# Kernel tuning notes

Hardware: AMD Instinct MI355X
Metric: run time of the kernel (lower is better)

## Reference

```python
import jax, jax.numpy as jnp
import numpy as np

C = 64   # in_channels
KS = 3   # kernel_size


def _wconv(p, W1, b1, W2, b2, W3, b3):
    # 1x1 conv stack: 3 -> 64 -> 256 -> C*KS*KS, ReLU between
    h = jax.nn.relu(jnp.einsum('oc,bchw->bohw', W1, p) + b1[None, :, None, None])
    h = jax.nn.relu(jnp.einsum('oc,bchw->bohw', W2, h) + b2[None, :, None, None])
    h = jnp.einsum('oc,bchw->bohw', W3, h) + b3[None, :, None, None]
    return h  # [1, C*KS*KS, ho, wo]


def setup_inputs() -> dict:
    key = jax.random.key(0)
    k = jax.random.split(key, 8)
    bs, hi, wi = 2, 128, 128
    ho, wo = 512, 512
    x = jax.random.normal(k[0], (bs, C, hi, wi), jnp.float32)
    poseMap = jax.random.normal(k[1], (1, 3, ho, wo), jnp.float32)
    interMapY = jax.random.randint(k[2], (ho, wo), 0, hi)
    interMapX = jax.random.randint(k[3], (ho, wo), 0, wi)
    W1 = jax.random.normal(k[4], (64, 3), jnp.float32) * 0.1
    b1 = jnp.zeros((64,), jnp.float32)
    W2 = jax.random.normal(k[5], (256, 64), jnp.float32) * 0.05
    b2 = jnp.zeros((256,), jnp.float32)
    W3 = jax.random.normal(k[6], (C * KS * KS, 256), jnp.float32) * 0.05
    b3 = jnp.zeros((C * KS * KS,), jnp.float32)
    return {'x': x, 'poseMap': poseMap, 'W1': W1, 'b1': b1, 'W2': W2, 'b2': b2,
            'W3': W3, 'b3': b3, 'interMapY': interMapY, 'interMapX': interMapX}


def reference(x, poseMap, W1, b1, W2, b2, W3, b3, interMapY, interMapX):
    bs, c, hi, wi = x.shape
    ho, wo = interMapY.shape
    # kernel prediction branch (poseMap is detached in the original)
    w = _wconv(jax.lax.stop_gradient(poseMap), W1, b1, W2, b2, W3, b3)
    w = w.reshape(C, KS * KS, ho, wo)
    sw = jax.nn.softmax(w, axis=1)  # softmax over the KS*KS taps
    # unfold(x, KS, padding=KS//2) tap k corresponds to xp[:, :, i + k//KS, j + k%KS]
    pad = KS // 2
    xp = jnp.pad(x, ((0, 0), (0, 0), (pad, pad), (pad, pad)))
    out = jnp.zeros((bs, C, ho, wo), x.dtype)
    for k in range(KS * KS):  # fixed small loop over taps; fuses gather+weight+reduce
        dy, dx = k // KS, k % KS
        g = xp[:, :, interMapY + dy, interMapX + dx]  # [bs, C, ho, wo] paired gather
        out = out + g * sw[None, :, k]  # sw[:, k] -> [C, ho, wo]
    return out
```

## Files before the change

### kernel.cpp

```cpp
#include <hip/hip_runtime.h>
#include <math.h>

#define HO 512
#define WO 512
#define HI 128
#define WI 128
#define CC 64
#define BS 2
#define NPX 64
#define NT 256

#define W2P_ELEMS (16 * 2 * 64 * 8)
#define W3P_ELEMS (36 * 8 * 64 * 8)
#define XT_ELEM_OFF (W2P_ELEMS + W3P_ELEMS)
#define XT_FLOATS (130 * 130 * 128)

typedef __attribute__((ext_vector_type(8))) short short8;
typedef __attribute__((ext_vector_type(4))) float float4v;

__device__ __forceinline__ unsigned short f2bf(float f) {
    unsigned u = __builtin_bit_cast(unsigned, f);
    unsigned r = (u + 0x7FFFu + ((u >> 16) & 1u)) >> 16;
    return (unsigned short)r;
}

__global__ void prepack_zw(const float* __restrict__ W2,
                           const float* __restrict__ W3,
                           unsigned short* __restrict__ wsp,
                           float* __restrict__ xt) {
    const int total = W2P_ELEMS + W3P_ELEMS;
    for (int idx = blockIdx.x * blockDim.x + threadIdx.x; idx < total;
         idx += gridDim.x * blockDim.x) {
        float v;
        if (idx < W2P_ELEMS) {
            int j = idx & 7, lane = (idx >> 3) & 63, rest = idx >> 9;
            int ks = rest & 1, nt = rest >> 1;
            int n = nt * 16 + (lane & 15);
            int k = ks * 32 + (lane >> 4) * 8 + j;
            v = W2[n * 64 + k];
        } else {
            int i2 = idx - W2P_ELEMS;
            int j = i2 & 7, lane = (i2 >> 3) & 63, rest = i2 >> 9;
            int ks = rest & 7, nt = rest >> 3;
            int tap = nt >> 2, ct = nt & 3;
            int row = (ct * 16 + (lane & 15)) * 9 + tap;
            int k = ks * 32 + (lane >> 4) * 8 + j;
            v = W3[row * 256 + k];
        }
        wsp[idx] = f2bf(v);
    }
    float4v z = {0.f, 0.f, 0.f, 0.f};
    float4v* xt4 = (float4v*)xt;
    for (int i = blockIdx.x * blockDim.x + threadIdx.x; i < XT_FLOATS / 4;
         i += gridDim.x * blockDim.x)
        xt4[i] = z;
}

__global__ void prepack_x(const float* __restrict__ x, float* __restrict__ xt) {
    const int tid = blockIdx.x * blockDim.x + threadIdx.x;
    const int pos = tid & 16383;
    const int g   = tid >> 14;
    const int h = pos >> 7, w = pos & 127;
    const float* src = x + pos;
    float4v v0, v1;
    #pragma unroll
    for (int j = 0; j < 4; ++j) v0[j] = src[(size_t)(g * 8 + j) * (HI * WI)];
    #pragma unroll
    for (int j = 0; j < 4; ++j) v1[j] = src[(size_t)(g * 8 + 4 + j) * (HI * WI)];
    float* dst = xt + ((h + 1) * 130 + (w + 1)) * 128 + g * 8;
    *(float4v*)dst = v0;
    *(float4v*)(dst + 4) = v1;
}

__global__ __launch_bounds__(NT, 3)
void fused_main(const float* __restrict__ xt, const float* __restrict__ pose,
                const float* __restrict__ W1, const float* __restrict__ b1,
                const float* __restrict__ b2, const float* __restrict__ b3,
                const int* __restrict__ iY, const int* __restrict__ iX,
                const unsigned short* __restrict__ wsp,
                float* __restrict__ out)
{
    __shared__ char smem[33792 + 17408 + 768 + 512];
    unsigned short (*sH2)[264] = (unsigned short (*)[264])&smem[0];
    unsigned short (*sH1)[72]  = (unsigned short (*)[72])&smem[33792];
    float (*sOut)[2][16][68]   = (float (*)[2][16][68])&smem[33792];
    float (*sP)[NPX]           = (float (*)[NPX])&smem[51200];
    int* sIY                   = (int*)&smem[51968];
    int* sIX                   = (int*)&smem[52224];

    const int t = threadIdx.x;
    const int pixBase = blockIdx.x * NPX;
    const int y  = pixBase / WO;
    const int x0 = pixBase % WO;

    if (t < 192) sP[t >> 6][t & 63] = pose[(t >> 6) * (HO * WO) + pixBase + (t & 63)];
    if (t < 64) sIY[t] = iY[pixBase + t];
    else if (t < 128) sIX[t - 64] = iX[pixBase + t - 64];
    __syncthreads();

    {
        const int p  = t & 63;
        const int og = t >> 6;
        const float p0 = sP[0][p], p1 = sP[1][p], p2 = sP[2][p];
        #pragma unroll
        for (int i = 0; i < 16; i += 2) {
            const int o = og * 16 + i;
            float a0 = fmaf(W1[o * 3 + 2], p2, fmaf(W1[o * 3 + 1], p1, fmaf(W1[o * 3 + 0], p0, b1[o])));
            float a1 = fmaf(W1[o * 3 + 5], p2, fmaf(W1[o * 3 + 4], p1, fmaf(W1[o * 3 + 3], p0, b1[o + 1])));
            a0 = fmaxf(a0, 0.f); a1 = fmaxf(a1, 0.f);
            unsigned pack = (unsigned)f2bf(a0) | ((unsigned)f2bf(a1) << 16);
            *(unsigned*)&sH1[p][o] = pack;
        }
    }
    __syncthreads();

    const int wv = t >> 6, l = t & 63, lm = l & 15, lq = l >> 4;
    const int m0 = wv * 16;

    {
        short8 a0 = *(const short8*)&sH1[m0 + lm][0  + lq * 8];
        short8 a1 = *(const short8*)&sH1[m0 + lm][32 + lq * 8];
        const short8* w2f = (const short8*)wsp;
        #pragma unroll 4
        for (int nt = 0; nt < 16; ++nt) {
            float4v acc = {0.f, 0.f, 0.f, 0.f};
            short8 bf0 = w2f[(nt * 2 + 0) * 64 + l];
            short8 bf1 = w2f[(nt * 2 + 1) * 64 + l];
            acc = __builtin_amdgcn_mfma_f32_16x16x32_bf16(a0, bf0, acc, 0, 0, 0);
            acc = __builtin_amdgcn_mfma_f32_16x16x32_bf16(a1, bf1, acc, 0, 0, 0);
            const float bv = b2[nt * 16 + lm];
            #pragma unroll
            for (int r = 0; r < 4; ++r)
                sH2[m0 + lq * 4 + r][nt * 16 + lm] = f2bf(fmaxf(acc[r] + bv, 0.f));
        }
    }
    __syncthreads();

    int pbase[4];
    #pragma unroll
    for (int r = 0; r < 4; ++r) {
        const int p = m0 + lq * 4 + r;
        pbase[r] = ((sIY[p] + 1) * 130 + (sIX[p] + 1)) * 128;
    }
    const int koff[9] = {-131 * 128, -130 * 128, -129 * 128,
                         -1 * 128,   0,          1 * 128,
                         129 * 128,  130 * 128,  131 * 128};
    const short8* w3f = (const short8*)(wsp + W2P_ELEMS);

    for (int ct = 0; ct < 4; ++ct) {
        float4v accs[9];
        #pragma unroll
        for (int tap = 0; tap < 9; ++tap) accs[tap] = (float4v){0.f, 0.f, 0.f, 0.f};

        #pragma unroll 2
        for (int ks = 0; ks < 8; ++ks) {
            short8 a = *(const short8*)&sH2[m0 + lm][ks * 32 + lq * 8];
            #pragma unroll
            for (int tap = 0; tap < 9; ++tap) {
                short8 b = w3f[(((tap << 2) | ct) * 8 + ks) * 64 + l];
                accs[tap] = __builtin_amdgcn_mfma_f32_16x16x32_bf16(a, b, accs[tap], 0, 0, 0);
            }
        }

        const int c = ct * 16 + lm;
        float bv[9];
        #pragma unroll
        for (int tap = 0; tap < 9; ++tap) bv[tap] = b3[c * 9 + tap];

        float ob0[4], ob1[4];
        #pragma unroll
        for (int r = 0; r < 4; ++r) {
            float lg[9];
            #pragma unroll
            for (int tap = 0; tap < 9; ++tap) lg[tap] = accs[tap][r] + bv[tap];
            float mx = lg[0];
            #pragma unroll
            for (int tap = 1; tap < 9; ++tap) mx = fmaxf(mx, lg[tap]);
            const float* xb = xt + pbase[r] + c;
            float s = 0.f, o0 = 0.f, o1 = 0.f;
            #pragma unroll
            for (int tap = 0; tap < 9; ++tap) {
                const float ev = __expf(lg[tap] - mx);
                s += ev;
                o0 = fmaf(ev, xb[koff[tap]], o0);
                o1 = fmaf(ev, xb[koff[tap] + 64], o1);
            }
            const float inv = 1.f / s;
            ob0[r] = o0 * inv;
            ob1[r] = o1 * inv;
        }

        float (*so)[16][68] = sOut[ct & 1];
        *(float4v*)&so[0][lm][m0 + lq * 4] = (float4v){ob0[0], ob0[1], ob0[2], ob0[3]};
        *(float4v*)&so[1][lm][m0 + lq * 4] = (float4v){ob1[0], ob1[1], ob1[2], ob1[3]};
        __syncthreads();

        const int row = t >> 3;
        const int b   = row >> 4, ch = row & 15;
        const int seg = (t & 7) * 8;
        float4v v0 = *(float4v*)&so[b][ch][seg];
        float4v v1 = *(float4v*)&so[b][ch][seg + 4];
        float* op = out + (((size_t)(b * CC + ct * 16 + ch) * HO) + y) * WO + x0 + seg;
        *(float4v*)op = v0;
        *(float4v*)(op + 4) = v1;
    }
}

extern "C" void kernel_launch(void* const* d_in, const int* in_sizes, int n_in,
                              void* d_out, int out_size, void* d_ws, size_t ws_size,
                              hipStream_t stream) {
    const float* x    = (const float*)d_in[0];
    const float* pose = (const float*)d_in[1];
    const float* W1   = (const float*)d_in[2];
    const float* b1   = (const float*)d_in[3];
    const float* W2   = (const float*)d_in[4];
    const float* b2   = (const float*)d_in[5];
    const float* W3   = (const float*)d_in[6];
    const float* b3   = (const float*)d_in[7];
    const int*   iY   = (const int*)d_in[8];
    const int*   iX   = (const int*)d_in[9];
    float* out = (float*)d_out;
    unsigned short* wsp = (unsigned short*)d_ws;
    float* xt = (float*)((char*)d_ws + XT_ELEM_OFF * sizeof(unsigned short));

    prepack_zw<<<2048, NT, 0, stream>>>(W2, W3, wsp, xt);
    prepack_x<<<1024, NT, 0, stream>>>(x, xt);

    const int nblocks = (HO * WO) / NPX;
    fused_main<<<nblocks, NT, 0, stream>>>(
        xt, pose, W1, b1, b2, b3, iY, iX, wsp, out);
}
```

Before: 425.0 us.

## Split third conv across waves by channel tile and shrink LDS footprint

Each wave now owns one 16-channel tile and computes all 64 pixels in two passes of two M-tiles, instead of every wave looping over four channel tiles for its own 16 pixels. Each W3 B-fragment load is reused for two MFMAs, and the W3 prepack layout is reordered to channel-tile-major to match. sH1, sH2 and sOut now share one LDS region, with an extra barrier after the H1 fragments are read into registers. Launch bounds rise to 4 blocks per CU. The trade-off is more live accumulators (18 float4) and per-thread output registers, which can cause spills under the tighter register budget.

```diff
diff --git a/kernel.cpp b/kernel.cpp
--- a/kernel.cpp
+++ b/kernel.cpp
@@ -42,7 +42,7 @@
             int i2 = idx - W2P_ELEMS;
             int j = i2 & 7, lane = (i2 >> 3) & 63, rest = i2 >> 9;
             int ks = rest & 7, nt = rest >> 3;
-            int tap = nt >> 2, ct = nt & 3;
+            int ct = nt / 9, tap = nt - ct * 9;
             int row = (ct * 16 + (lane & 15)) * 9 + tap;
             int k = ks * 32 + (lane >> 4) * 8 + j;
             v = W3[row * 256 + k];
@@ -72,7 +72,7 @@
     *(float4v*)(dst + 4) = v1;
 }
 
-__global__ __launch_bounds__(NT, 3)
+__global__ __launch_bounds__(NT, 4)
 void fused_main(const float* __restrict__ xt, const float* __restrict__ pose,
                 const float* __restrict__ W1, const float* __restrict__ b1,
                 const float* __restrict__ b2, const float* __restrict__ b3,
@@ -80,13 +80,13 @@
                 const unsigned short* __restrict__ wsp,
                 float* __restrict__ out)
 {
-    __shared__ char smem[33792 + 17408 + 768 + 512];
+    __shared__ char smem[34816 + 768 + 256 + 256];
+    unsigned short (*sH1)[72]  = (unsigned short (*)[72])&smem[0];
     unsigned short (*sH2)[264] = (unsigned short (*)[264])&smem[0];
-    unsigned short (*sH1)[72]  = (unsigned short (*)[72])&smem[33792];
-    float (*sOut)[2][16][68]   = (float (*)[2][16][68])&smem[33792];
-    float (*sP)[NPX]           = (float (*)[NPX])&smem[51200];
-    int* sIY                   = (int*)&smem[51968];
-    int* sIX                   = (int*)&smem[52224];
+    float (*sOut)[2][16][68]   = (float (*)[2][16][68])&smem[0];
+    float (*sP)[NPX]           = (float (*)[NPX])&smem[34816];
+    int* sIY                   = (int*)&smem[35584];
+    int* sIX                   = (int*)&smem[35840];
 
     const int t = threadIdx.x;
     const int pixBase = blockIdx.x * NPX;
@@ -117,17 +117,19 @@
     const int wv = t >> 6, l = t & 63, lm = l & 15, lq = l >> 4;
     const int m0 = wv * 16;
 
+    short8 h1a0 = *(const short8*)&sH1[m0 + lm][0  + lq * 8];
+    short8 h1a1 = *(const short8*)&sH1[m0 + lm][32 + lq * 8];
+    __syncthreads();
+
     {
-        short8 a0 = *(const short8*)&sH1[m0 + lm][0  + lq * 8];
-        short8 a1 = *(const short8*)&sH1[m0 + lm][32 + lq * 8];
         const short8* w2f = (const short8*)wsp;
         #pragma unroll 4
         for (int nt = 0; nt < 16; ++nt) {
             float4v acc = {0.f, 0.f, 0.f, 0.f};
             short8 bf0 = w2f[(nt * 2 + 0) * 64 + l];
             short8 bf1 = w2f[(nt * 2 + 1) * 64 + l];
-            acc = __builtin_amdgcn_mfma_f32_16x16x32_bf16(a0, bf0, acc, 0, 0, 0);
-            acc = __builtin_amdgcn_mfma_f32_16x16x32_bf16(a1, bf1, acc, 0, 0, 0);
+            acc = __builtin_amdgcn_mfma_f32_16x16x32_bf16(h1a0, bf0, acc, 0, 0, 0);
+            acc = __builtin_amdgcn_mfma_f32_16x16x32_bf16(h1a1, bf1, acc, 0, 0, 0);
             const float bv = b2[nt * 16 + lm];
             #pragma unroll
             for (int r = 0; r < 4; ++r)
@@ -136,73 +138,86 @@
     }
     __syncthreads();
 
-    int pbase[4];
-    #pragma unroll
-    for (int r = 0; r < 4; ++r) {
-        const int p = m0 + lq * 4 + r;
-        pbase[r] = ((sIY[p] + 1) * 130 + (sIX[p] + 1)) * 128;
-    }
+    const int c = wv * 16 + lm;
+    const short8* w3w = ((const short8*)(wsp + W2P_ELEMS)) + (size_t)wv * (9 * 8 * 64);
     const int koff[9] = {-131 * 128, -130 * 128, -129 * 128,
                          -1 * 128,   0,          1 * 128,
                          129 * 128,  130 * 128,  131 * 128};
-    const short8* w3f = (const short8*)(wsp + W2P_ELEMS);
-
-    for (int ct = 0; ct < 4; ++ct) {
-        float4v accs[9];
-        #pragma unroll
-        for (int tap = 0; tap < 9; ++tap) accs[tap] = (float4v){0.f, 0.f, 0.f, 0.f};
-
+    float bv[9];
+    #pragma unroll
+    for (int tap = 0; tap < 9; ++tap) bv[tap] = b3[c * 9 + tap];
+
+    float oreg[2][2][4][2];
+
+    #pragma unroll
+    for (int pass = 0; pass < 2; ++pass) {
+        float4v acc0[9], acc1[9];
+        #pragma unroll
+        for (int tap = 0; tap < 9; ++tap) {
+            acc0[tap] = (float4v){0.f, 0.f, 0.f, 0.f};
+            acc1[tap] = (float4v){0.f, 0.f, 0.f, 0.f};
+        }
         #pragma unroll 2
         for (int ks = 0; ks < 8; ++ks) {
-            short8 a = *(const short8*)&sH2[m0 + lm][ks * 32 + lq * 8];
+            short8 a0 = *(const short8*)&sH2[pass * 32 + lm][ks * 32 + lq * 8];
+            short8 a1 = *(const short8*)&sH2[pass * 32 + 16 + lm][ks * 32 + lq * 8];
             #pragma unroll
             for (int tap = 0; tap < 9; ++tap) {
-                short8 b = w3f[(((tap << 2) | ct) * 8 + ks) * 64 + l];
-                accs[tap] = __builtin_amdgcn_mfma_f32_16x16x32_bf16(a, b, accs[tap], 0, 0, 0);
+                short8 b = w3w[(tap * 8 + ks) * 64 + l];
+                acc0[tap] = __builtin_amdgcn_mfma_f32_16x16x32_bf16(a0, b, acc0[tap], 0, 0, 0);
+                acc1[tap] = __builtin_amdgcn_mfma_f32_16x16x32_bf16(a1, b, acc1[tap], 0, 0, 0);
             }
         }
-
-        const int c = ct * 16 + lm;
-        float bv[9];
-        #pragma unroll
-        for (int tap = 0; tap < 9; ++tap) bv[tap] = b3[c * 9 + tap];
-
-        float ob0[4], ob1[4];
-        #pragma unroll
-        for (int r = 0; r < 4; ++r) {
-            float lg[9];
-            #pragma unroll
-            for (int tap = 0; tap < 9; ++tap) lg[tap] = accs[tap][r] + bv[tap];
-            float mx = lg[0];
-            #pragma unroll
-            for (int tap = 1; tap < 9; ++tap) mx = fmaxf(mx, lg[tap]);
-            const float* xb = xt + pbase[r] + c;
-            float s = 0.f, o0 = 0.f, o1 = 0.f;
-            #pragma unroll
-            for (int tap = 0; tap < 9; ++tap) {
-                const float ev = __expf(lg[tap] - mx);
-                s += ev;
-                o0 = fmaf(ev, xb[koff[tap]], o0);
-                o1 = fmaf(ev, xb[koff[tap] + 64], o1);
+        #pragma unroll
+        for (int mt = 0; mt < 2; ++mt) {
+            #pragma unroll
+            for (int r = 0; r < 4; ++r) {
+                const int px = pass * 32 + mt * 16 + lq * 4 + r;
+                float lg[9];
+                #pragma unroll
+                for (int tap = 0; tap < 9; ++tap)
+                    lg[tap] = (mt == 0 ? acc0[tap][r] : acc1[tap][r]) + bv[tap];
+                float mx = lg[0];
+                #pragma unroll
+                for (int tap = 1; tap < 9; ++tap) mx = fmaxf(mx, lg[tap]);
+                const float* xb = xt + ((sIY[px] + 1) * 130 + (sIX[px] + 1)) * 128 + c;
+                float s = 0.f, o0 = 0.f, o1 = 0.f;
+                #pragma unroll
+                for (int tap = 0; tap < 9; ++tap) {
+                    const float ev = __expf(lg[tap] - mx);
+                    s += ev;
+                    o0 = fmaf(ev, xb[koff[tap]], o0);
+                    o1 = fmaf(ev, xb[koff[tap] + 64], o1);
+                }
+                const float inv = 1.f / s;
+                oreg[pass][mt][r][0] = o0 * inv;
+                oreg[pass][mt][r][1] = o1 * inv;
             }
-            const float inv = 1.f / s;
-            ob0[r] = o0 * inv;
-            ob1[r] = o1 * inv;
-        }
-
-        float (*so)[16][68] = sOut[ct & 1];
-        *(float4v*)&so[0][lm][m0 + lq * 4] = (float4v){ob0[0], ob0[1], ob0[2], ob0[3]};
-        *(float4v*)&so[1][lm][m0 + lq * 4] = (float4v){ob1[0], ob1[1], ob1[2], ob1[3]};
-        __syncthreads();
-
-        const int row = t >> 3;
-        const int b   = row >> 4, ch = row & 15;
-        const int seg = (t & 7) * 8;
-        float4v v0 = *(float4v*)&so[b][ch][seg];
-        float4v v1 = *(float4v*)&so[b][ch][seg + 4];
-        float* op = out + (((size_t)(b * CC + ct * 16 + ch) * HO) + y) * WO + x0 + seg;
-        *(float4v*)op = v0;
-        *(float4v*)(op + 4) = v1;
+        }
+    }
+
+    __syncthreads();
+
+    #pragma unroll
+    for (int pass = 0; pass < 2; ++pass)
+        #pragma unroll
+        for (int mt = 0; mt < 2; ++mt)
+            #pragma unroll
+            for (int b = 0; b < 2; ++b)
+                *(float4v*)&sOut[wv][b][lm][pass * 32 + mt * 16 + lq * 4] =
+                    (float4v){oreg[pass][mt][0][b], oreg[pass][mt][1][b],
+                              oreg[pass][mt][2][b], oreg[pass][mt][3][b]};
+    __syncthreads();
+
+    {
+        const int row = t >> 1, half = t & 1;
+        const int wvp = row >> 5, bb = (row >> 4) & 1, ch = row & 15;
+        const float* sop = &sOut[wvp][bb][ch][half * 32];
+        float* op = out + (((size_t)(bb * CC + wvp * 16 + ch) * HO) + y) * WO
+                    + x0 + half * 32;
+        #pragma unroll
+        for (int k = 0; k < 8; ++k)
+            *(float4v*)&op[k * 4] = *(const float4v*)&sop[k * 4];
     }
 }
 
```

After: 1.313 ms. +209.1%, slower.
